# Kernel optimization log

Measured on AMD Instinct MI355X. Metric: run time of the kernel, lower is better.

## Reference

```python
import jax, jax.numpy as jnp
import numpy as np

EPS = 1e-5
NUM_GROUPS = 32
NUM_HEADS = 4


def setup_inputs() -> dict:
    key = jax.random.key(0)
    ks = jax.random.split(key, 3)
    B, C, H, W = 4, 256, 64, 64
    x = jax.random.normal(ks[0], (B, C, H, W), dtype=jnp.float32)
    gn_w = jnp.ones((C,), jnp.float32)
    gn_b = jnp.zeros((C,), jnp.float32)
    qkv_w = jax.random.normal(ks[1], (3 * C, C), dtype=jnp.float32) * (C ** -0.5)
    qkv_b = jnp.zeros((3 * C,), jnp.float32)
    proj_w = jax.random.normal(ks[2], (C, C), dtype=jnp.float32) * (C ** -0.5)
    proj_b = jnp.zeros((C,), jnp.float32)
    return {"x": x, "gn_w": gn_w, "gn_b": gn_b, "qkv_w": qkv_w,
            "qkv_b": qkv_b, "proj_w": proj_w, "proj_b": proj_b}


def _group_norm(x, w, b):
    B, C, H, W = x.shape
    xg = x.reshape(B, NUM_GROUPS, C // NUM_GROUPS, H, W)
    mean = xg.mean(axis=(2, 3, 4), keepdims=True)
    var = xg.var(axis=(2, 3, 4), keepdims=True)
    xn = ((xg - mean) * jax.lax.rsqrt(var + EPS)).reshape(B, C, H, W)
    return xn * w[None, :, None, None] + b[None, :, None, None]


def reference(x, gn_w, gn_b, qkv_w, qkv_b, proj_w, proj_b):
    B, C, H, W = x.shape
    nh = NUM_HEADS
    d = C // nh
    L = H * W
    h = _group_norm(x, gn_w, gn_b)
    # 1x1 conv == channel matmul
    qkv = jnp.einsum('oc,bchw->bohw', qkv_w, h) + qkv_b[None, :, None, None]
    q, k, v = jnp.split(qkv, 3, axis=1)
    # (B, C, H, W) -> (B, nh, L, d)
    def to_heads(t):
        return t.reshape(B, nh, d, L).transpose(0, 1, 3, 2)
    q, k, v = to_heads(q), to_heads(k), to_heads(v)
    scale = d ** -0.5
    attn = jax.nn.softmax(jnp.einsum('bhqd,bhkd->bhqk', q, k) * scale, axis=-1)
    o = jnp.einsum('bhqk,bhkd->bhqd', attn, v)          # (B, nh, L, d)
    o = o.transpose(0, 1, 3, 2).reshape(B, C, H, W)
    o = jnp.einsum('oc,bchw->bohw', proj_w, o) + proj_b[None, :, None, None]
    return x + o
```

## Files before the change

kernel.cpp:

```cpp
#include <hip/hip_runtime.h>

#define B_   4
#define C_   256
#define L_   4096
#define NH_  4
#define D_   64
#define G_   32
#define CPG_ 8

typedef __bf16 bf16x8 __attribute__((ext_vector_type(8)));
typedef float  f32x4  __attribute__((ext_vector_type(4)));

__device__ __forceinline__ ushort f2bf(float f) {
  union { float f; unsigned u; } c; c.f = f;
  unsigned u = c.u;
  return (ushort)((u + 0x7fffu + ((u >> 16) & 1u)) >> 16);
}
__device__ __forceinline__ float bf2f(ushort h) {
  union { unsigned u; float f; } c; c.u = ((unsigned)h) << 16; return c.f;
}
__device__ __forceinline__ unsigned fbits(float f) {
  union { float f; unsigned u; } c; c.f = f; return c.u;
}
__device__ __forceinline__ float fastexp2(float x) {
#if __has_builtin(__builtin_amdgcn_exp2f)
  return __builtin_amdgcn_exp2f(x);
#else
  return exp2f(x);
#endif
}

__global__ __launch_bounds__(256) void cvt_kernel(const float* __restrict__ wq,
                                                  const float* __restrict__ wp,
                                                  ushort* __restrict__ oq,
                                                  ushort* __restrict__ op,
                                                  float* __restrict__ stats) {
  int t = blockIdx.x * 256 + threadIdx.x;
  if (blockIdx.x == 0) stats[threadIdx.x] = 0.f;
  const int NQ4 = (768 * 256) / 4;
  float4 v;
  if (t < NQ4) {
    v = ((const float4*)wq)[t];
    ((ushort4*)oq)[t] = make_ushort4(f2bf(v.x), f2bf(v.y), f2bf(v.z), f2bf(v.w));
  } else {
    int i = t - NQ4;
    v = ((const float4*)wp)[i];
    ((ushort4*)op)[i] = make_ushort4(f2bf(v.x), f2bf(v.y), f2bf(v.z), f2bf(v.w));
  }
}

__global__ __launch_bounds__(256) void gn_stats(const float* __restrict__ x,
                                                float* __restrict__ stats) {
  int bg = blockIdx.x >> 3, chunk = blockIdx.x & 7;
  int b = bg >> 5, g = bg & 31;
  const float* xg = x + ((size_t)b * C_ + g * CPG_) * L_ + chunk * 512;
  int tid = threadIdx.x;

  float s = 0.f, ss = 0.f;
  for (int c = 0; c < CPG_; ++c) {
    float2 v = ((const float2*)(xg + (size_t)c * L_))[tid];
    s  += v.x + v.y;
    ss += v.x * v.x + v.y * v.y;
  }
  for (int off = 32; off; off >>= 1) { s += __shfl_xor(s, off); ss += __shfl_xor(ss, off); }
  __shared__ float red[8];
  int w = tid >> 6;
  if ((tid & 63) == 0) { red[w] = s; red[4 + w] = ss; }
  __syncthreads();
  if (tid == 0) {
    atomicAdd(&stats[bg * 2],     red[0] + red[1] + red[2] + red[3]);
    atomicAdd(&stats[bg * 2 + 1], red[4] + red[5] + red[6] + red[7]);
  }
}

__global__ __launch_bounds__(256) void gn_apply(const float* __restrict__ x,
                                                const float* __restrict__ gw,
                                                const float* __restrict__ gb,
                                                const float* __restrict__ stats,
                                                ushort* __restrict__ hT) {
  int bg = blockIdx.x >> 3, chunk = blockIdx.x & 7;
  int b = bg >> 5, g = bg & 31;
  const float* xg = x + ((size_t)b * C_ + g * CPG_) * L_;
  int tid = threadIdx.x;

  const float inv_n = 1.0f / (CPG_ * L_);
  float mean = stats[bg * 2] * inv_n;
  float var  = stats[bg * 2 + 1] * inv_n - mean * mean;
  float rstd = rsqrtf(var + 1e-5f);

  float wv[CPG_], bv[CPG_];
  for (int c = 0; c < CPG_; ++c) { wv[c] = gw[g * CPG_ + c]; bv[c] = gb[g * CPG_ + c]; }

  for (int li = 0; li < 2; ++li) {
    int l = chunk * 512 + li * 256 + tid;
    union { ushort s[8]; uint4 u; } o;
    for (int c = 0; c < CPG_; ++c) {
      float v = xg[(size_t)c * L_ + l];
      o.s[c] = f2bf((v - mean) * rstd * wv[c] + bv[c]);
    }
    *(uint4*)(hT + ((size_t)b * L_ + l) * C_ + g * CPG_) = o.u;
  }
}

__global__ __launch_bounds__(256) void qkv_kernel(const ushort* __restrict__ hT,
                                                  const ushort* __restrict__ w,
                                                  const float* __restrict__ bias,
                                                  ushort* __restrict__ q,
                                                  ushort* __restrict__ k,
                                                  ushort* __restrict__ v) {
  int wid  = blockIdx.x * 4 + (threadIdx.x >> 6);
  int lane = threadIdx.x & 63;
  int quad = lane >> 4, col = lane & 15;
  int ot   = wid % 12;
  int rest = wid / 12;
  int lt   = rest & 127;
  int b    = rest >> 7;
  int o0 = ot * 64, l0 = lt * 32;

  const ushort* abase = w  + (size_t)(o0 + col) * C_ + quad * 8;
  const ushort* bbase = hT + ((size_t)b * L_ + l0 + col) * C_ + quad * 8;

  f32x4 acc[4][2];
  for (int i = 0; i < 4; ++i) for (int j = 0; j < 2; ++j)
    acc[i][j] = (f32x4){0.f, 0.f, 0.f, 0.f};

#pragma unroll
  for (int k0 = 0; k0 < C_; k0 += 32) {
    bf16x8 a[4], bb[2];
#pragma unroll
    for (int i = 0; i < 4; ++i) a[i]  = *(const bf16x8*)(abase + (size_t)(i * 16) * C_ + k0);
#pragma unroll
    for (int j = 0; j < 2; ++j) bb[j] = *(const bf16x8*)(bbase + (size_t)(j * 16) * C_ + k0);
#pragma unroll
    for (int i = 0; i < 4; ++i)
#pragma unroll
      for (int j = 0; j < 2; ++j)
        acc[i][j] = __builtin_amdgcn_mfma_f32_16x16x32_bf16(a[i], bb[j], acc[i][j], 0, 0, 0);
  }

  int third = o0 >> 8;
  int hh    = (o0 & 255) >> 6;
  float scale = (third == 0) ? 0.180336880111120f : 1.0f;
#pragma unroll
  for (int i = 0; i < 4; ++i) {
    int oo = o0 + i * 16 + quad * 4;
    int dd = i * 16 + quad * 4;
#pragma unroll
    for (int j = 0; j < 2; ++j) {
      int l = l0 + j * 16 + col;
      ushort pk[4];
      for (int r = 0; r < 4; ++r) pk[r] = f2bf((acc[i][j][r] + bias[oo + r]) * scale);
      if (third < 2) {
        ushort* dst = (third ? k : q) + (((size_t)(b * NH_ + hh) * L_ + l) * D_ + dd);
        *(ushort4*)dst = make_ushort4(pk[0], pk[1], pk[2], pk[3]);
      } else {
        for (int r = 0; r < 4; ++r)
          v[((size_t)(b * NH_ + hh) * D_ + dd + r) * L_ + l] = pk[r];
      }
    }
  }
}

__global__ __launch_bounds__(256, 2) void attn_kernel(const ushort* __restrict__ q,
                                                      const ushort* __restrict__ k,
                                                      const ushort* __restrict__ v,
                                                      ushort* __restrict__ p0,
                                                      ushort* __restrict__ p1,
                                                      float* __restrict__ psumbuf) {
  __shared__ __align__(16) ushort k_lds[2][64][72];
  __shared__ __align__(16) ushort v_lds[2][64][72];

  int tid   = threadIdx.x;
  int w     = tid >> 6, lane = tid & 63;
  int quad  = lane >> 4, col = lane & 15;
  int bid   = (int)blockIdx.x;
  bid = (bid & 7) * 64 + (bid >> 3);
  int split = bid >> 8;
  int bh    = (bid >> 4) & 15;
  int qblk  = bid & 15;

  const ushort* qp = q + (size_t)bh * L_ * D_;
  const ushort* kp = k + (size_t)bh * L_ * D_;
  const ushort* vp = v + (size_t)bh * D_ * L_;

  int qrow0 = qblk * 256 + w * 64;
  bf16x8 bq[4][2];
#pragma unroll
  for (int f = 0; f < 4; ++f)
#pragma unroll
    for (int c = 0; c < 2; ++c)
      bq[f][c] = *(const bf16x8*)(qp + (size_t)(qrow0 + f * 16 + col) * D_ + c * 32 + quad * 8);

  f32x4 oacc[4][4];
#pragma unroll
  for (int f = 0; f < 4; ++f)
    for (int t = 0; t < 4; ++t) oacc[f][t] = (f32x4){0.f, 0.f, 0.f, 0.f};
  float psum[4] = {0.f, 0.f, 0.f, 0.f};
  const f32x4 Z = (f32x4){0.f, 0.f, 0.f, 0.f};

  int vrow = tid >> 2, vchunk = tid & 3;
  int vwoff = (vchunk >> 1) * 32 + (vchunk & 1) * 4;
  int kt0 = split * (L_ / 2), kt_end = kt0 + L_ / 2;

  {
    const uint4* ksrc = (const uint4*)(kp + (size_t)kt0 * D_);
    uint4 a  = ksrc[tid];
    uint4 b2 = ksrc[tid + 256];
    const uint4* vsrc = (const uint4*)(vp + (size_t)vrow * L_ + kt0);
    uint4 c0 = vsrc[vchunk * 2];
    uint4 c1 = vsrc[vchunk * 2 + 1];
    *(uint4*)&k_lds[0][tid >> 3][(tid & 7) * 8] = a;
    *(uint4*)&k_lds[0][32 + (tid >> 3)][(tid & 7) * 8] = b2;
    ushort* vb = &v_lds[0][vrow][vwoff];
    *(uint2*)(vb + 0)  = make_uint2(c0.x, c0.y);
    *(uint2*)(vb + 8)  = make_uint2(c0.z, c0.w);
    *(uint2*)(vb + 16) = make_uint2(c1.x, c1.y);
    *(uint2*)(vb + 24) = make_uint2(c1.z, c1.w);
  }
  __syncthreads();

  int cur = 0;
  for (int kt = kt0; kt < kt_end; kt += 64) {
    bool has_next = (kt + 64) < kt_end;

    f32x4 s[2][4][2];
#pragma unroll
    for (int h = 0; h < 2; ++h) {
      bf16x8 a00 = *(const bf16x8*)&k_lds[cur][h * 32 + col][quad * 8];
      bf16x8 a01 = *(const bf16x8*)&k_lds[cur][h * 32 + col][32 + quad * 8];
      bf16x8 a10 = *(const bf16x8*)&k_lds[cur][h * 32 + 16 + col][quad * 8];
      bf16x8 a11 = *(const bf16x8*)&k_lds[cur][h * 32 + 16 + col][32 + quad * 8];
#pragma unroll
      for (int f = 0; f < 4; ++f) {
        s[h][f][0] = __builtin_amdgcn_mfma_f32_16x16x32_bf16(a00, bq[f][0], Z, 0, 0, 0);
        s[h][f][1] = __builtin_amdgcn_mfma_f32_16x16x32_bf16(a10, bq[f][0], Z, 0, 0, 0);
        s[h][f][0] = __builtin_amdgcn_mfma_f32_16x16x32_bf16(a01, bq[f][1], s[h][f][0], 0, 0, 0);
        s[h][f][1] = __builtin_amdgcn_mfma_f32_16x16x32_bf16(a11, bq[f][1], s[h][f][1], 0, 0, 0);
      }
    }

    uint4 nk0, nk1, nv0, nv1;
    if (has_next) {
      const uint4* ksrc = (const uint4*)(kp + (size_t)(kt + 64) * D_);
      nk0 = ksrc[tid];
      nk1 = ksrc[tid + 256];
      const uint4* vsrc = (const uint4*)(vp + (size_t)vrow * L_ + (kt + 64));
      nv0 = vsrc[vchunk * 2];
      nv1 = vsrc[vchunk * 2 + 1];
    }

#pragma unroll
    for (int h = 0; h < 2; ++h) {
      bf16x8 pb[4];
#pragma unroll
      for (int f = 0; f < 4; ++f) {
        float pe0[4], pe1[4];
#pragma unroll
        for (int r = 0; r < 4; ++r) {
          pe0[r] = fastexp2(s[h][f][0][r]);
          pe1[r] = fastexp2(s[h][f][1][r]);
        }
        psum[f] += ((pe0[0] + pe0[1]) + (pe0[2] + pe0[3])) +
                   ((pe1[0] + pe1[1]) + (pe1[2] + pe1[3]));
        union { unsigned u[4]; bf16x8 v8; } pc;
        pc.u[0] = __builtin_amdgcn_perm(fbits(pe0[1]), fbits(pe0[0]), 0x07060302u);
        pc.u[1] = __builtin_amdgcn_perm(fbits(pe0[3]), fbits(pe0[2]), 0x07060302u);
        pc.u[2] = __builtin_amdgcn_perm(fbits(pe1[1]), fbits(pe1[0]), 0x07060302u);
        pc.u[3] = __builtin_amdgcn_perm(fbits(pe1[3]), fbits(pe1[2]), 0x07060302u);
        pb[f] = pc.v8;
      }
#pragma unroll
      for (int t = 0; t < 4; ++t) {
        bf16x8 av = *(const bf16x8*)&v_lds[cur][t * 16 + col][h * 32 + quad * 8];
#pragma unroll
        for (int f = 0; f < 4; ++f)
          oacc[f][t] = __builtin_amdgcn_mfma_f32_16x16x32_bf16(av, pb[f], oacc[f][t], 0, 0, 0);
      }
    }

    if (has_next) {
      int nb = cur ^ 1;
      *(uint4*)&k_lds[nb][tid >> 3][(tid & 7) * 8] = nk0;
      *(uint4*)&k_lds[nb][32 + (tid >> 3)][(tid & 7) * 8] = nk1;
      ushort* vb = &v_lds[nb][vrow][vwoff];
      *(uint2*)(vb + 0)  = make_uint2(nv0.x, nv0.y);
      *(uint2*)(vb + 8)  = make_uint2(nv0.z, nv0.w);
      *(uint2*)(vb + 16) = make_uint2(nv1.x, nv1.y);
      *(uint2*)(vb + 24) = make_uint2(nv1.z, nv1.w);
      __syncthreads();
      cur = nb;
    }
  }

  ushort* po = split ? p1 : p0;
#pragma unroll
  for (int f = 0; f < 4; ++f) {
    psum[f] += __shfl_xor(psum[f], 16);
    psum[f] += __shfl_xor(psum[f], 32);
    for (int t = 0; t < 4; ++t) {
      ushort ok[4];
      for (int r = 0; r < 4; ++r) ok[r] = f2bf(oacc[f][t][r]);
      ushort* dst = po + ((size_t)bh * L_ + qrow0 + f * 16 + col) * D_ + t * 16 + quad * 4;
      *(ushort4*)dst = make_ushort4(ok[0], ok[1], ok[2], ok[3]);
    }
    if (quad == 0)
      psumbuf[split * (16 * L_) + bh * L_ + qrow0 + f * 16 + col] = psum[f];
  }
}

__global__ __launch_bounds__(256) void comb_kernel(ushort* __restrict__ p0,
                                                   const ushort* __restrict__ p1,
                                                   const float* __restrict__ ps) {
  int idx = blockIdx.x * 256 + threadIdx.x;
  int row = idx >> 4;
  float inv = 1.0f / (ps[row] + ps[16 * L_ + row]);
  ushort4 a = ((const ushort4*)p0)[idx];
  ushort4 b = ((const ushort4*)p1)[idx];
  ((ushort4*)p0)[idx] = make_ushort4(
      f2bf((bf2f(a.x) + bf2f(b.x)) * inv),
      f2bf((bf2f(a.y) + bf2f(b.y)) * inv),
      f2bf((bf2f(a.z) + bf2f(b.z)) * inv),
      f2bf((bf2f(a.w) + bf2f(b.w)) * inv));
}

__global__ __launch_bounds__(256) void proj_kernel(const ushort* __restrict__ oin,
                                                   const ushort* __restrict__ pw,
                                                   const float* __restrict__ pb,
                                                   const float* __restrict__ x,
                                                   float* __restrict__ out) {
  int wid  = blockIdx.x * 4 + (threadIdx.x >> 6);
  int lane = threadIdx.x & 63;
  int quad = lane >> 4, col = lane & 15;
  int oct  = wid & 7;
  int rest = wid >> 3;
  int lt   = rest & 127;
  int b    = rest >> 7;
  int l0 = lt * 32, oc0 = oct * 32;

  f32x4 acc[2][2];
  for (int i = 0; i < 2; ++i) for (int j = 0; j < 2; ++j)
    acc[i][j] = (f32x4){0.f, 0.f, 0.f, 0.f};

#pragma unroll
  for (int k0 = 0; k0 < C_; k0 += 32) {
    int hh = k0 >> 6, dk = k0 & 63;
    bf16x8 a[2], bb[2];
#pragma unroll
    for (int i = 0; i < 2; ++i)
      a[i] = *(const bf16x8*)(oin + ((size_t)(b * NH_ + hh) * L_ + l0 + i * 16 + col) * D_ + dk + quad * 8);
#pragma unroll
    for (int j = 0; j < 2; ++j)
      bb[j] = *(const bf16x8*)(pw + (size_t)(oc0 + j * 16 + col) * C_ + k0 + quad * 8);
#pragma unroll
    for (int i = 0; i < 2; ++i)
#pragma unroll
      for (int j = 0; j < 2; ++j)
        acc[i][j] = __builtin_amdgcn_mfma_f32_16x16x32_bf16(a[i], bb[j], acc[i][j], 0, 0, 0);
  }

#pragma unroll
  for (int j = 0; j < 2; ++j) {
    int oc = oc0 + j * 16 + col;
    float bias = pb[oc];
#pragma unroll
    for (int i = 0; i < 2; ++i) {
      int l = l0 + i * 16 + quad * 4;
      size_t off = ((size_t)b * C_ + oc) * L_ + l;
      float4 xv = *(const float4*)(x + off);
      float4 ov = make_float4(acc[i][j][0] + bias + xv.x,
                              acc[i][j][1] + bias + xv.y,
                              acc[i][j][2] + bias + xv.z,
                              acc[i][j][3] + bias + xv.w);
      *(float4*)(out + off) = ov;
    }
  }
}

extern "C" void kernel_launch(void* const* d_in, const int* in_sizes, int n_in,
                              void* d_out, int out_size, void* d_ws, size_t ws_size,
                              hipStream_t stream) {
  const float* x      = (const float*)d_in[0];
  const float* gn_w   = (const float*)d_in[1];
  const float* gn_b   = (const float*)d_in[2];
  const float* qkv_w  = (const float*)d_in[3];
  const float* qkv_b  = (const float*)d_in[4];
  const float* proj_w = (const float*)d_in[5];
  const float* proj_b = (const float*)d_in[6];
  float* out = (float*)d_out;

  const size_t TEN = (size_t)B_ * C_ * L_;
  ushort* ws  = (ushort*)d_ws;
  ushort* q   = ws;
  ushort* k   = ws + TEN;
  ushort* v   = ws + 2 * TEN;
  ushort* oat = ws + 3 * TEN;
  ushort* wq  = ws + 4 * TEN;
  ushort* wp  = wq + 768 * 256;
  float*  stats = (float*)(wp + 256 * 256);
  ushort* hT  = (ushort*)d_out;
  ushort* p1  = (ushort*)d_out + TEN;
  float*  psb = (float*)d_out;

  cvt_kernel <<<256,       256, 0, stream>>>(qkv_w, proj_w, wq, wp, stats);
  gn_stats   <<<1024,      256, 0, stream>>>(x, stats);
  gn_apply   <<<1024,      256, 0, stream>>>(x, gn_w, gn_b, stats, hT);
  qkv_kernel <<<6144 / 4,  256, 0, stream>>>(hT, wq, qkv_b, q, k, v);
  attn_kernel<<<512,       256, 0, stream>>>(q, k, v, oat, p1, psb);
  comb_kernel<<<4096,      256, 0, stream>>>(oat, p1, psb);
  proj_kernel<<<4096 / 4,  256, 0, stream>>>(oat, wp, proj_b, x, out);
}
```

Measured before the change: 219.0 us.

## Fuse weight conversion with GN stats, MFMA row sums, widen combine kernel

The weight-conversion and group-norm statistics kernels are merged into one launch. Per-chunk partial sums are now written directly instead of atomically accumulated, and gn_apply reduces the 8 partials itself. The attention kernel computes softmax row sums with an extra MFMA against a ones vector instead of VALU adds and shuffles. The combine kernel processes 8 elements per thread with half the blocks. Together these cut launch count, atomics and VALU work in the attention inner loop, at the cost of four extra MFMAs per half-step and row sums taken from bf16-rounded probabilities.

```diff
diff --git a/kernel.cpp b/kernel.cpp
--- a/kernel.cpp
+++ b/kernel.cpp
@@ -30,31 +30,31 @@
 #endif
 }
 
-__global__ __launch_bounds__(256) void cvt_kernel(const float* __restrict__ wq,
-                                                  const float* __restrict__ wp,
-                                                  ushort* __restrict__ oq,
-                                                  ushort* __restrict__ op,
-                                                  float* __restrict__ stats) {
-  int t = blockIdx.x * 256 + threadIdx.x;
-  if (blockIdx.x == 0) stats[threadIdx.x] = 0.f;
-  const int NQ4 = (768 * 256) / 4;
-  float4 v;
-  if (t < NQ4) {
-    v = ((const float4*)wq)[t];
-    ((ushort4*)oq)[t] = make_ushort4(f2bf(v.x), f2bf(v.y), f2bf(v.z), f2bf(v.w));
-  } else {
-    int i = t - NQ4;
-    v = ((const float4*)wp)[i];
-    ((ushort4*)op)[i] = make_ushort4(f2bf(v.x), f2bf(v.y), f2bf(v.z), f2bf(v.w));
-  }
-}
-
-__global__ __launch_bounds__(256) void gn_stats(const float* __restrict__ x,
-                                                float* __restrict__ stats) {
-  int bg = blockIdx.x >> 3, chunk = blockIdx.x & 7;
+__global__ __launch_bounds__(256) void pre_kernel(const float* __restrict__ x,
+                                                  const float* __restrict__ wqf,
+                                                  const float* __restrict__ wpf,
+                                                  ushort* __restrict__ wq,
+                                                  ushort* __restrict__ wp,
+                                                  float* __restrict__ stats2) {
+  int bidx = blockIdx.x;
+  int tid  = threadIdx.x;
+  if (bidx >= 1024) {
+    int t = (bidx - 1024) * 256 + tid;
+    const int NQ4 = (768 * 256) / 4;
+    float4 v;
+    if (t < NQ4) {
+      v = ((const float4*)wqf)[t];
+      ((ushort4*)wq)[t] = make_ushort4(f2bf(v.x), f2bf(v.y), f2bf(v.z), f2bf(v.w));
+    } else {
+      int i = t - NQ4;
+      v = ((const float4*)wpf)[i];
+      ((ushort4*)wp)[i] = make_ushort4(f2bf(v.x), f2bf(v.y), f2bf(v.z), f2bf(v.w));
+    }
+    return;
+  }
+  int bg = bidx >> 3, chunk = bidx & 7;
   int b = bg >> 5, g = bg & 31;
   const float* xg = x + ((size_t)b * C_ + g * CPG_) * L_ + chunk * 512;
-  int tid = threadIdx.x;
 
   float s = 0.f, ss = 0.f;
   for (int c = 0; c < CPG_; ++c) {
@@ -68,24 +68,30 @@
   if ((tid & 63) == 0) { red[w] = s; red[4 + w] = ss; }
   __syncthreads();
   if (tid == 0) {
-    atomicAdd(&stats[bg * 2],     red[0] + red[1] + red[2] + red[3]);
-    atomicAdd(&stats[bg * 2 + 1], red[4] + red[5] + red[6] + red[7]);
+    stats2[bidx * 2]     = red[0] + red[1] + red[2] + red[3];
+    stats2[bidx * 2 + 1] = red[4] + red[5] + red[6] + red[7];
   }
 }
 
 __global__ __launch_bounds__(256) void gn_apply(const float* __restrict__ x,
                                                 const float* __restrict__ gw,
                                                 const float* __restrict__ gb,
-                                                const float* __restrict__ stats,
+                                                const float* __restrict__ stats2,
                                                 ushort* __restrict__ hT) {
   int bg = blockIdx.x >> 3, chunk = blockIdx.x & 7;
   int b = bg >> 5, g = bg & 31;
   const float* xg = x + ((size_t)b * C_ + g * CPG_) * L_;
   int tid = threadIdx.x;
 
+  float s = 0.f, ss = 0.f;
+#pragma unroll
+  for (int c2 = 0; c2 < 8; ++c2) {
+    s  += stats2[(bg * 8 + c2) * 2];
+    ss += stats2[(bg * 8 + c2) * 2 + 1];
+  }
   const float inv_n = 1.0f / (CPG_ * L_);
-  float mean = stats[bg * 2] * inv_n;
-  float var  = stats[bg * 2 + 1] * inv_n - mean * mean;
+  float mean = s * inv_n;
+  float var  = ss * inv_n - mean * mean;
   float rstd = rsqrtf(var + 1e-5f);
 
   float wv[CPG_], bv[CPG_];
@@ -195,8 +201,15 @@
 #pragma unroll
   for (int f = 0; f < 4; ++f)
     for (int t = 0; t < 4; ++t) oacc[f][t] = (f32x4){0.f, 0.f, 0.f, 0.f};
-  float psum[4] = {0.f, 0.f, 0.f, 0.f};
+  f32x4 pacc[4];
+#pragma unroll
+  for (int f = 0; f < 4; ++f) pacc[f] = (f32x4){0.f, 0.f, 0.f, 0.f};
   const f32x4 Z = (f32x4){0.f, 0.f, 0.f, 0.f};
+
+  union { ushort s[8]; bf16x8 v8; } one_u;
+#pragma unroll
+  for (int i = 0; i < 8; ++i) one_u.s[i] = 0x3F80;
+  bf16x8 ones = one_u.v8;
 
   int vrow = tid >> 2, vchunk = tid & 3;
   int vwoff = (vchunk >> 1) * 32 + (vchunk & 1) * 4;
@@ -260,8 +273,6 @@
           pe0[r] = fastexp2(s[h][f][0][r]);
           pe1[r] = fastexp2(s[h][f][1][r]);
         }
-        psum[f] += ((pe0[0] + pe0[1]) + (pe0[2] + pe0[3])) +
-                   ((pe1[0] + pe1[1]) + (pe1[2] + pe1[3]));
         union { unsigned u[4]; bf16x8 v8; } pc;
         pc.u[0] = __builtin_amdgcn_perm(fbits(pe0[1]), fbits(pe0[0]), 0x07060302u);
         pc.u[1] = __builtin_amdgcn_perm(fbits(pe0[3]), fbits(pe0[2]), 0x07060302u);
@@ -269,6 +280,9 @@
         pc.u[3] = __builtin_amdgcn_perm(fbits(pe1[3]), fbits(pe1[2]), 0x07060302u);
         pb[f] = pc.v8;
       }
+#pragma unroll
+      for (int f = 0; f < 4; ++f)
+        pacc[f] = __builtin_amdgcn_mfma_f32_16x16x32_bf16(ones, pb[f], pacc[f], 0, 0, 0);
 #pragma unroll
       for (int t = 0; t < 4; ++t) {
         bf16x8 av = *(const bf16x8*)&v_lds[cur][t * 16 + col][h * 32 + quad * 8];
@@ -295,8 +309,6 @@
   ushort* po = split ? p1 : p0;
 #pragma unroll
   for (int f = 0; f < 4; ++f) {
-    psum[f] += __shfl_xor(psum[f], 16);
-    psum[f] += __shfl_xor(psum[f], 32);
     for (int t = 0; t < 4; ++t) {
       ushort ok[4];
       for (int r = 0; r < 4; ++r) ok[r] = f2bf(oacc[f][t][r]);
@@ -304,7 +316,7 @@
       *(ushort4*)dst = make_ushort4(ok[0], ok[1], ok[2], ok[3]);
     }
     if (quad == 0)
-      psumbuf[split * (16 * L_) + bh * L_ + qrow0 + f * 16 + col] = psum[f];
+      psumbuf[split * (16 * L_) + bh * L_ + qrow0 + f * 16 + col] = pacc[f][0];
   }
 }
 
@@ -312,15 +324,15 @@
                                                    const ushort* __restrict__ p1,
                                                    const float* __restrict__ ps) {
   int idx = blockIdx.x * 256 + threadIdx.x;
-  int row = idx >> 4;
+  int row = idx >> 3;
   float inv = 1.0f / (ps[row] + ps[16 * L_ + row]);
-  ushort4 a = ((const ushort4*)p0)[idx];
-  ushort4 b = ((const ushort4*)p1)[idx];
-  ((ushort4*)p0)[idx] = make_ushort4(
-      f2bf((bf2f(a.x) + bf2f(b.x)) * inv),
-      f2bf((bf2f(a.y) + bf2f(b.y)) * inv),
-      f2bf((bf2f(a.z) + bf2f(b.z)) * inv),
-      f2bf((bf2f(a.w) + bf2f(b.w)) * inv));
+  union { uint4 u; ushort s[8]; } ua, ub, o;
+  ua.u = ((const uint4*)p0)[idx];
+  ub.u = ((const uint4*)p1)[idx];
+#pragma unroll
+  for (int e = 0; e < 8; ++e)
+    o.s[e] = f2bf((bf2f(ua.s[e]) + bf2f(ub.s[e])) * inv);
+  ((uint4*)p0)[idx] = o.u;
 }
 
 __global__ __launch_bounds__(256) void proj_kernel(const ushort* __restrict__ oin,
@@ -396,16 +408,15 @@
   ushort* oat = ws + 3 * TEN;
   ushort* wq  = ws + 4 * TEN;
   ushort* wp  = wq + 768 * 256;
-  float*  stats = (float*)(wp + 256 * 256);
   ushort* hT  = (ushort*)d_out;
   ushort* p1  = (ushort*)d_out + TEN;
+  float*  st2 = (float*)((ushort*)d_out + TEN);
   float*  psb = (float*)d_out;
 
-  cvt_kernel <<<256,       256, 0, stream>>>(qkv_w, proj_w, wq, wp, stats);
-  gn_stats   <<<1024,      256, 0, stream>>>(x, stats);
-  gn_apply   <<<1024,      256, 0, stream>>>(x, gn_w, gn_b, stats, hT);
+  pre_kernel <<<1280,      256, 0, stream>>>(x, qkv_w, proj_w, wq, wp, st2);
+  gn_apply   <<<1024,      256, 0, stream>>>(x, gn_w, gn_b, st2, hT);
   qkv_kernel <<<6144 / 4,  256, 0, stream>>>(hT, wq, qkv_b, q, k, v);
   attn_kernel<<<512,       256, 0, stream>>>(q, k, v, oat, p1, psb);
-  comb_kernel<<<4096,      256, 0, stream>>>(oat, p1, psb);
+  comb_kernel<<<2048,      256, 0, stream>>>(oat, p1, psb);
   proj_kernel<<<4096 / 4,  256, 0, stream>>>(oat, wp, proj_b, x, out);
 }
```

After: 211.0 us. 1.04x faster.
